# Kernel tuning notes

Hardware: AMD Instinct MI355X
Metric: run time of the kernel (lower is better)

## Reference

```python
import jax, jax.numpy as jnp
import numpy as np

N_USER = 50000
N_ITEM = 50000
E = 800000
C_IN = 128
C_OUT = 128
N_HEADS = 4


def setup_inputs() -> dict:
    key = jax.random.key(0)
    ks = jax.random.split(key, 12)
    xav = lambda k, shp: jax.random.uniform(k, shp, jnp.float32, -1.0, 1.0) * jnp.sqrt(6.0 / (shp[0] + shp[1]))
    return {
        'x_user': jax.random.normal(ks[0], (N_USER, C_IN), jnp.float32),
        'x_item': jax.random.normal(ks[1], (N_ITEM, C_IN), jnp.float32),
        'ei_u2i': jnp.stack([jax.random.randint(ks[2], (E,), 0, N_USER, jnp.int32),
                             jax.random.randint(ks[3], (E,), 0, N_ITEM, jnp.int32)]),
        'ei_i2u': jnp.stack([jax.random.randint(ks[4], (E,), 0, N_ITEM, jnp.int32),
                             jax.random.randint(ks[5], (E,), 0, N_USER, jnp.int32)]),
        'W_nb': xav(ks[6], (C_OUT, C_IN)),
        'b_nb': jnp.zeros((C_OUT,), jnp.float32),
        'W_self': xav(ks[7], (C_OUT, C_IN)),
        'b_self': jnp.zeros((C_OUT,), jnp.float32),
        'in_proj_w': xav(ks[8], (3 * C_OUT, C_OUT)),
        'in_proj_b': jnp.zeros((3 * C_OUT,), jnp.float32),
        'out_proj_w': xav(ks[9], (C_OUT, C_OUT)),
        'out_proj_b': jnp.zeros((C_OUT,), jnp.float32),
    }


def _multi_aggr(h_src, edge_index, n_dst):
    """h_src: already lin_neighbor-transformed src features [N_src, C].
    Returns [n_dst, 4, C] stacked as [max, min, sum, mean] (torch_scatter semantics:
    empty segments -> 0; mean divides by clamp(count, 1))."""
    src, dst = edge_index[0], edge_index[1]
    msgs = h_src[src]  # [E, C]  (linear commutes with gather)
    s = jax.ops.segment_sum(msgs, dst, num_segments=n_dst)
    cnt = jax.ops.segment_sum(jnp.ones((msgs.shape[0],), msgs.dtype), dst, num_segments=n_dst)
    has = (cnt > 0)[:, None]
    mean = s / jnp.maximum(cnt, 1.0)[:, None]
    mx = jnp.where(has, jax.ops.segment_max(msgs, dst, num_segments=n_dst), 0.0)
    mn = jnp.where(has, jax.ops.segment_min(msgs, dst, num_segments=n_dst), 0.0)
    return jnp.stack([mx, mn, s, mean], axis=1)  # [n_dst, 4, C]


def _mha(tokens, in_proj_w, in_proj_b, out_proj_w, out_proj_b):
    """torch nn.MultiheadAttention (eval mode, batch_first=False). tokens: [S, N, C]."""
    S, N, C = tokens.shape
    H, Dh = N_HEADS, C // N_HEADS
    qkv = tokens @ in_proj_w.T + in_proj_b            # [S, N, 3C]
    q, k, v = jnp.split(qkv, 3, axis=-1)
    q = q.reshape(S, N, H, Dh) * (1.0 / jnp.sqrt(jnp.asarray(Dh, tokens.dtype)))
    k = k.reshape(S, N, H, Dh)
    v = v.reshape(S, N, H, Dh)
    scores = jnp.einsum('snhd,tnhd->nhst', q, k)       # [N, H, S, S]
    attn = jax.nn.softmax(scores, axis=-1)
    o = jnp.einsum('nhst,tnhd->snhd', attn, v).reshape(S, N, C)
    return o @ out_proj_w.T + out_proj_b               # [S, N, C]


def reference(x_user, x_item, ei_u2i, ei_i2u, W_nb, b_nb, W_self, b_self,
              in_proj_w, in_proj_b, out_proj_w, out_proj_b):
    # shared neighbor linear applied once per node type, then gathered per edge
    h_user = x_user @ W_nb.T + b_nb
    h_item = x_item @ W_nb.T + b_nb
    aggr_item = _multi_aggr(h_user, ei_u2i, N_ITEM)    # user->item : [N_item, 4, C]
    aggr_user = _multi_aggr(h_item, ei_i2u, N_USER)    # item->user : [N_user, 4, C]

    def per_type(x, aggr):
        self_feat = x @ W_self.T + b_self              # [N, C]
        # tokens: [self, max, min, sum, mean] -> [5, N, C]
        tokens = jnp.concatenate([self_feat[None], jnp.transpose(aggr, (1, 0, 2))], axis=0)
        attn_out = _mha(tokens, in_proj_w, in_proj_b, out_proj_w, out_proj_b)
        return self_feat + attn_out.mean(axis=0)

    out_user = per_type(x_user, aggr_user)
    out_item = per_type(x_item, aggr_item)
    return (out_user, out_item)
```

## Files before the change

kernel.cpp:

```cpp
#include <hip/hip_runtime.h>
#include <hip/hip_bf16.h>


#define C 128
#define NHEAD 4
#define DH 32
#define QK_SCALE 0.17677669529663687f

typedef __attribute__((ext_vector_type(8))) short bf16x8;
typedef __attribute__((ext_vector_type(4))) short short4v;
typedef __attribute__((ext_vector_type(2))) short short2v;
typedef __attribute__((ext_vector_type(4))) float f32x4;

__device__ __forceinline__ short f2bf(float f) {
    unsigned u = __float_as_uint(f);
    unsigned r = u + 0x7FFFu + ((u >> 16) & 1u);
    return (short)(r >> 16);
}

__global__ __launch_bounds__(256, 2) void transform_prep_kernel(
    const float* __restrict__ xu, const float* __restrict__ xi,
    int NU, int NTOT,
    const float* __restrict__ Wnb, const float* __restrict__ bnb,
    const float* __restrict__ Wself, const float* __restrict__ bself,
    unsigned short* __restrict__ h_bf, unsigned short* __restrict__ self_bf,
    float* __restrict__ selfout,
    const float* __restrict__ Wip, unsigned* __restrict__ img,
    int* __restrict__ curA, int nA, int* __restrict__ curB, int nB, int TB)
{
    const int tid = threadIdx.x;

    if ((int)blockIdx.x >= TB) {
        int bid2 = (int)blockIdx.x - TB;
        if (bid2 < 96) {
            int id = bid2 * 256 + tid;
            int ks = id / (384 * 16);
            int rem = id - ks * (384 * 16);
            int n = rem >> 4, kk = rem & 15;
            float a = Wip[(size_t)n * C + ks * 32 + kk * 2 + 0];
            float b = Wip[(size_t)n * C + ks * 32 + kk * 2 + 1];
            unsigned pa = ((unsigned)(unsigned short)f2bf(a))
                        | (((unsigned)(unsigned short)f2bf(b)) << 16);
            img[(size_t)ks * 6144 + n * 16 + kk] = pa;
        } else {
            int i = (bid2 - 96) * 256 + tid;
            if (i < nA) curA[i] = 0;
            else if (i < nA + nB) curB[i - nA] = 0;
        }
        return;
    }

    __shared__ float As[64 * 132];
    __shared__ float Bs[256 * 36];
    __shared__ float biasS[256];

    const int row0 = blockIdx.x * 64;

    biasS[tid] = (tid < 128) ? bnb[tid] : bself[tid - 128];

#pragma unroll
    for (int i = 0; i < 8; i++) {
        int id = tid + i * 256;
        int r = id >> 5, c4 = id & 31;
        int row = row0 + r;
        float4 v = make_float4(0.f, 0.f, 0.f, 0.f);
        if (row < NTOT) {
            v = (row < NU) ? ((const float4*)xu)[(size_t)row * 32 + c4]
                           : ((const float4*)xi)[(size_t)(row - NU) * 32 + c4];
        }
        *(float4*)&As[r * 132 + c4 * 4] = v;
    }

    const int tm = tid >> 5;
    const int tn = tid & 31;

    float acc[8][8];
#pragma unroll
    for (int m = 0; m < 8; m++)
#pragma unroll
        for (int j = 0; j < 8; j++) acc[m][j] = 0.f;

    for (int ks = 0; ks < 4; ks++) {
        __syncthreads();
#pragma unroll
        for (int i = 0; i < 8; i++) {
            int id = tid + i * 256;
            int n = id >> 3, q = id & 7;
            const float4* src = (n < 128)
                ? &((const float4*)Wnb)[(size_t)n * 32 + ks * 8 + q]
                : &((const float4*)Wself)[(size_t)(n - 128) * 32 + ks * 8 + q];
            *(float4*)&Bs[n * 36 + q * 4] = *src;
        }
        __syncthreads();

        for (int k4 = 0; k4 < 8; k4++) {
            float4 a[8];
#pragma unroll
            for (int m = 0; m < 8; m++)
                a[m] = *(const float4*)&As[(tm * 8 + m) * 132 + ks * 32 + k4 * 4];
            float4 b[8];
#pragma unroll
            for (int j = 0; j < 8; j++)
                b[j] = *(const float4*)&Bs[(tn + 32 * j) * 36 + k4 * 4];
#pragma unroll
            for (int m = 0; m < 8; m++) {
                float4 av = a[m];
#pragma unroll
                for (int j = 0; j < 8; j++) {
                    float4 bv = b[j];
                    acc[m][j] += av.x * bv.x + av.y * bv.y
                               + av.z * bv.z + av.w * bv.w;
                }
            }
        }
    }

#pragma unroll
    for (int m = 0; m < 8; m++) {
        int row = row0 + tm * 8 + m;
        if (row < NTOT) {
#pragma unroll
            for (int j = 0; j < 8; j++) {
                int jj = tn + 32 * j;
                float v = acc[m][j] + biasS[jj];
                if (j < 4) {
                    h_bf[(size_t)row * C + jj] = (unsigned short)f2bf(v);
                } else {
                    selfout[(size_t)row * C + (jj - 128)] = v;
                    self_bf[(size_t)row * C + (jj - 128)] = (unsigned short)f2bf(v);
                }
            }
        }
    }
}

__global__ __launch_bounds__(256) void hist2_kernel(
    const int* __restrict__ dstA, int nA, int* __restrict__ curA,
    const int* __restrict__ dstB, int nB, int* __restrict__ curB)
{
    int i = blockIdx.x * 256 + threadIdx.x;
    if (i < nA) atomicAdd(&curA[dstA[i]], 1);
    else if (i < nA + nB) atomicAdd(&curB[dstB[i - nA]], 1);
}

__global__ __launch_bounds__(1024) void scan2_kernel(
    int* __restrict__ curA, int nA, int* __restrict__ curB, int nB)
{
    int* cur = (blockIdx.x == 0) ? curA : curB;
    const int n = (blockIdx.x == 0) ? nA : nB;

    __shared__ int wsum[16];
    __shared__ int carryS;
    const int tid = threadIdx.x, lane = tid & 63, wv = tid >> 6;
    if (tid == 0) carryS = 0;
    __syncthreads();
    for (int base = 0; base < n; base += 4096) {
        int i0 = base + tid * 4;
        int v0 = 0, v1 = 0, v2 = 0, v3 = 0;
        if (i0 + 3 < n) {
            int4 t = *(const int4*)&cur[i0];
            v0 = t.x; v1 = t.y; v2 = t.z; v3 = t.w;
        } else {
            if (i0 < n) v0 = cur[i0];
            if (i0 + 1 < n) v1 = cur[i0 + 1];
            if (i0 + 2 < n) v2 = cur[i0 + 2];
            if (i0 + 3 < n) v3 = cur[i0 + 3];
        }
        int s1 = v0 + v1, s2 = s1 + v2, s3 = s2 + v3;
        int x = s3;
#pragma unroll
        for (int d = 1; d < 64; d <<= 1) {
            int t = __shfl_up(x, d, 64);
            if (lane >= d) x += t;
        }
        if (lane == 63) wsum[wv] = x;
        int carry = carryS;
        __syncthreads();
        int wpre = 0;
#pragma unroll
        for (int w2 = 0; w2 < 16; w2++) wpre += (w2 < wv) ? wsum[w2] : 0;
        int excl = x - s3 + wpre + carry;
        if (i0 + 3 < n) {
            int4 st; st.x = excl; st.y = excl + v0; st.z = excl + s1; st.w = excl + s2;
            *(int4*)&cur[i0] = st;
        } else {
            if (i0 < n) cur[i0] = excl;
            if (i0 + 1 < n) cur[i0 + 1] = excl + v0;
            if (i0 + 2 < n) cur[i0 + 2] = excl + s1;
            if (i0 + 3 < n) cur[i0 + 3] = excl + s2;
        }
        __syncthreads();
        if (tid == 0) {
            int t = 0;
#pragma unroll
            for (int w2 = 0; w2 < 16; w2++) t += wsum[w2];
            carryS = carry + t;
        }
        __syncthreads();
    }
}

__global__ __launch_bounds__(256) void fill2_kernel(
    const int* __restrict__ srcA, const int* __restrict__ dstA, int nA,
    int* __restrict__ curA, unsigned short* __restrict__ csrA,
    const int* __restrict__ srcB, const int* __restrict__ dstB, int nB,
    int* __restrict__ curB, unsigned short* __restrict__ csrB)
{
    int i = blockIdx.x * 256 + threadIdx.x;
    if (i < nA) {
        int p = atomicAdd(&curA[dstA[i]], 1);
        csrA[p] = (unsigned short)srcA[i];
    } else if (i < nA + nB) {
        int j = i - nA;
        int p = atomicAdd(&curB[dstB[j]], 1);
        csrB[p] = (unsigned short)srcB[j];
    }
}

#define ATN 4

__global__ __launch_bounds__(256, 8) void attn_fused_kernel(
    const unsigned short* __restrict__ h_bf, const unsigned short* __restrict__ csr,
    const int* __restrict__ cur, const unsigned short* __restrict__ self_bf,
    const short* __restrict__ wipbf, const float* __restrict__ bip,
    float* __restrict__ omean_g, int n_nodes)
{
    __shared__ char Ash[16 * 272];
    __shared__ float cinv[ATN];

    const int tid = threadIdx.x;
    const int lane = tid & 63;
    const int wv = tid >> 6;
    const int node0 = blockIdx.x * ATN;

    if (tid < 128) {
        int r = tid >> 5, c4 = tid & 31;
        int node = node0 + r;
        short4v b = {0, 0, 0, 0};
        if (node < n_nodes)
            b = *(const short4v*)(self_bf + (size_t)node * C + c4 * 4);
        *(short4v*)(Ash + (r * 4) * 272 + c4 * 8) = b;
    }

    {
        const unsigned* h2 = (const unsigned*)h_bf;
        int node = node0 + wv;
        float2 vs = make_float2(0.f, 0.f);
        float2 vmx = make_float2(-3.4e38f, -3.4e38f);
        float2 vmn = make_float2(3.4e38f, 3.4e38f);
        int deg = 0;
        if (node < n_nodes) {
            int start = (node == 0) ? 0 : cur[node - 1];
            int end = cur[node];
            deg = end - start;
            int e = start;
            for (; e + 8 <= end; e += 8) {
                unsigned v[8];
#pragma unroll
                for (int i = 0; i < 8; i++) {
                    int s = csr[e + i];
                    v[i] = h2[(size_t)s * 64 + lane];
                }
#pragma unroll
                for (int i = 0; i < 8; i++) {
                    float fx = __uint_as_float(v[i] << 16);
                    float fy = __uint_as_float(v[i] & 0xFFFF0000u);
                    vs.x += fx; vs.y += fy;
                    vmx.x = fmaxf(vmx.x, fx); vmx.y = fmaxf(vmx.y, fy);
                    vmn.x = fminf(vmn.x, fx); vmn.y = fminf(vmn.y, fy);
                }
            }
            if (e < end) {
                int last = end - 1;
                unsigned v[8];
#pragma unroll
                for (int i = 0; i < 8; i++) {
                    int idx = e + i;
                    int s = csr[(idx <= last) ? idx : last];
                    v[i] = h2[(size_t)s * 64 + lane];
                }
#pragma unroll
                for (int i = 0; i < 8; i++) {
                    if (e + i <= last) {
                        float fx = __uint_as_float(v[i] << 16);
                        float fy = __uint_as_float(v[i] & 0xFFFF0000u);
                        vs.x += fx; vs.y += fy;
                        vmx.x = fmaxf(vmx.x, fx); vmx.y = fmaxf(vmx.y, fy);
                        vmn.x = fminf(vmn.x, fx); vmn.y = fminf(vmn.y, fy);
                    }
                }
            }
        }
        if (deg == 0) {
            vmx = make_float2(0.f, 0.f);
            vmn = make_float2(0.f, 0.f);
        }
        short2v p;
        p.x = f2bf(vmx.x); p.y = f2bf(vmx.y);
        *(short2v*)(Ash + (wv * 4 + 1) * 272 + lane * 4) = p;
        p.x = f2bf(vmn.x); p.y = f2bf(vmn.y);
        *(short2v*)(Ash + (wv * 4 + 2) * 272 + lane * 4) = p;
        p.x = f2bf(vs.x); p.y = f2bf(vs.y);
        *(short2v*)(Ash + (wv * 4 + 3) * 272 + lane * 4) = p;
        if (lane == 0) cinv[wv] = 1.f / (float)max(deg, 1);
    }
    __syncthreads();

    const int quad = lane >> 4;
    const int col16 = lane & 15;

    f32x4 acc[6];
#pragma unroll
    for (int t = 0; t < 6; t++) acc[t] = (f32x4){0.f, 0.f, 0.f, 0.f};

#pragma unroll
    for (int ks = 0; ks < 4; ks++) {
        bf16x8 af = *(const bf16x8*)(Ash + col16 * 272 + ks * 64 + quad * 16);
#pragma unroll
        for (int t = 0; t < 6; t++) {
            int nb = wv * 32 + (t & 1) * 16 + (t >> 1) * 128 + col16;
            bf16x8 bfr = *(const bf16x8*)((const char*)wipbf
                          + (size_t)ks * 24576 + (size_t)nb * 64 + quad * 16);
            acc[t] = __builtin_amdgcn_mfma_f32_16x16x32_bf16(af, bfr, acc[t], 0, 0, 0);
        }
    }

    const float ci = cinv[quad];
    const float cis = ci * QK_SCALE;

    const float bq0 = bip[wv * 32 + col16];
    const float bq1 = bip[wv * 32 + 16 + col16];
    const float bk0 = bip[128 + wv * 32 + col16];
    const float bk1 = bip[128 + wv * 32 + 16 + col16];
    const float bv0 = bip[256 + wv * 32 + col16];
    const float bv1 = bip[256 + wv * 32 + 16 + col16];
    const float bq0s = bq0 * QK_SCALE;
    const float bq1s = bq1 * QK_SCALE;

    float k0[5], k1[5];
#pragma unroll
    for (int s = 0; s < 4; s++) { k0[s] = acc[2][s] + bk0; k1[s] = acc[3][s] + bk1; }
    k0[4] = fmaf(acc[2][3], ci, bk0);
    k1[4] = fmaf(acc[3][3], ci, bk1);

    float wj[5] = {0.f, 0.f, 0.f, 0.f, 0.f};
#pragma unroll
    for (int i = 0; i < 5; i++) {
        float qi0 = (i < 4) ? fmaf(acc[0][i], QK_SCALE, bq0s)
                            : fmaf(acc[0][3], cis, bq0s);
        float qi1 = (i < 4) ? fmaf(acc[1][i], QK_SCALE, bq1s)
                            : fmaf(acc[1][3], cis, bq1s);
        float sv[5];
#pragma unroll
        for (int j = 0; j < 5; j++) sv[j] = qi0 * k0[j] + qi1 * k1[j];
#pragma unroll
        for (int j = 0; j < 5; j++) {
            sv[j] += __shfl_xor(sv[j], 1, 16);
            sv[j] += __shfl_xor(sv[j], 2, 16);
            sv[j] += __shfl_xor(sv[j], 4, 16);
            sv[j] += __shfl_xor(sv[j], 8, 16);
        }
        float m = sv[0];
#pragma unroll
        for (int j = 1; j < 5; j++) m = fmaxf(m, sv[j]);
        float e[5], l = 0.f;
#pragma unroll
        for (int j = 0; j < 5; j++) { e[j] = __expf(sv[j] - m); l += e[j]; }
        float inv = 0.2f / l;
#pragma unroll
        for (int j = 0; j < 5; j++) wj[j] = fmaf(e[j], inv, wj[j]);
    }

    float o0 = 0.f, o1 = 0.f;
#pragma unroll
    for (int j = 0; j < 5; j++) {
        float v0 = (j < 4) ? (acc[4][j] + bv0) : fmaf(acc[4][3], ci, bv0);
        float v1 = (j < 4) ? (acc[5][j] + bv1) : fmaf(acc[5][3], ci, bv1);
        o0 = fmaf(wj[j], v0, o0);
        o1 = fmaf(wj[j], v1, o1);
    }

    int node = node0 + quad;
    if (node < n_nodes) {
        omean_g[(size_t)node * C + wv * 32 + col16] = o0;
        omean_g[(size_t)node * C + wv * 32 + 16 + col16] = o1;
    }
}

__global__ __launch_bounds__(256, 3) void outproj_kernel(
    const float* __restrict__ omean_g, const float* __restrict__ Wop,
    const float* __restrict__ bop, float* __restrict__ out, int M)
{
    __shared__ float As[64 * 132];
    __shared__ float Bs[128 * 36];
    __shared__ float bopS[C];

    const int tid = threadIdx.x;
    const int m0 = blockIdx.x * 64;

    if (tid < C) bopS[tid] = bop[tid];

#pragma unroll
    for (int i = 0; i < 8; i++) {
        int id = tid + i * 256;
        int r = id >> 5, c4 = id & 31;
        float4 v = make_float4(0.f, 0.f, 0.f, 0.f);
        if (m0 + r < M) v = ((const float4*)omean_g)[(size_t)(m0 + r) * 32 + c4];
        *(float4*)&As[r * 132 + c4 * 4] = v;
    }

    const int tn = tid & 31;
    const int tm = tid >> 5;
    float acc[8][4];
#pragma unroll
    for (int m = 0; m < 8; m++)
#pragma unroll
        for (int j = 0; j < 4; j++) acc[m][j] = 0.f;

    for (int ks = 0; ks < 4; ks++) {
        __syncthreads();
#pragma unroll
        for (int i = 0; i < 4; i++) {
            int id = tid + i * 256;
            int n = id >> 3, q = id & 7;
            float4 w = ((const float4*)Wop)[(size_t)n * 32 + ks * 8 + q];
            *(float4*)&Bs[n * 36 + q * 4] = w;
        }
        __syncthreads();

        for (int k4 = 0; k4 < 8; k4++) {
            float4 a[8];
#pragma unroll
            for (int m = 0; m < 8; m++)
                a[m] = *(const float4*)&As[(tm * 8 + m) * 132 + ks * 32 + k4 * 4];
            float4 b[4];
#pragma unroll
            for (int j = 0; j < 4; j++)
                b[j] = *(const float4*)&Bs[(tn + 32 * j) * 36 + k4 * 4];
#pragma unroll
            for (int m = 0; m < 8; m++) {
                float4 av = a[m];
#pragma unroll
                for (int j = 0; j < 4; j++) {
                    float4 bv = b[j];
                    acc[m][j] += av.x * bv.x + av.y * bv.y
                               + av.z * bv.z + av.w * bv.w;
                }
            }
        }
    }

#pragma unroll
    for (int m = 0; m < 8; m++) {
        int row = m0 + tm * 8 + m;
        if (row < M) {
#pragma unroll
            for (int j = 0; j < 4; j++) {
                int col = tn + 32 * j;
                float* o = &out[(size_t)row * C + col];
                *o += acc[m][j] + bopS[col];
            }
        }
    }
}

extern "C" void kernel_launch(void* const* d_in, const int* in_sizes, int n_in,
                              void* d_out, int out_size, void* d_ws, size_t ws_size,
                              hipStream_t stream) {
    const float* x_user = (const float*)d_in[0];
    const float* x_item = (const float*)d_in[1];
    const int*   ei_u2i = (const int*)d_in[2];
    const int*   ei_i2u = (const int*)d_in[3];
    const float* W_nb   = (const float*)d_in[4];
    const float* b_nb   = (const float*)d_in[5];
    const float* W_self = (const float*)d_in[6];
    const float* b_self = (const float*)d_in[7];
    const float* Wip    = (const float*)d_in[8];
    const float* bip    = (const float*)d_in[9];
    const float* Wop    = (const float*)d_in[10];
    const float* bop    = (const float*)d_in[11];

    const int NU = in_sizes[0] / C;
    const int NI = in_sizes[1] / C;
    const int E1 = in_sizes[2] / 2;
    const int E2 = in_sizes[3] / 2;
    const int NTOT = NU + NI;

    float* out_user = (float*)d_out;
    float* out_item = out_user + (size_t)NU * C;

    float* ws = (float*)d_ws;
    short* wipbf            = (short*)ws;
    unsigned short* h_bf    = (unsigned short*)(ws + 24576);
    const size_t rc = (size_t)NTOT * C;
    unsigned short* self_bf = h_bf + rc;
    float* omean_all        = (float*)(self_bf + rc);
    int*   curA             = (int*)(omean_all + rc);
    int*   curB             = curA + NI;
    unsigned short* csrA16  = (unsigned short*)(curB + NU);
    unsigned short* csrB16  = csrA16 + E1;

    unsigned short* h_user_bf = h_bf;
    unsigned short* h_item_bf = h_bf + (size_t)NU * C;
    unsigned short* self_user_bf = self_bf;
    unsigned short* self_item_bf = self_bf + (size_t)NU * C;
    float* om_user = omean_all;
    float* om_item = omean_all + (size_t)NU * C;

    const int TB = (NTOT + 63) / 64;
    const int PB = 96 + (NTOT + 255) / 256;
    transform_prep_kernel<<<TB + PB, 256, 0, stream>>>(
        x_user, x_item, NU, NTOT, W_nb, b_nb, W_self, b_self,
        h_bf, self_bf, (float*)d_out, Wip, (unsigned*)wipbf,
        curA, NI, curB, NU, TB);

    hist2_kernel<<<(E1 + E2 + 255) / 256, 256, 0, stream>>>(
        ei_u2i + E1, E1, curA, ei_i2u + E2, E2, curB);

    scan2_kernel<<<2, 1024, 0, stream>>>(curA, NI, curB, NU);

    fill2_kernel<<<(E1 + E2 + 255) / 256, 256, 0, stream>>>(
        ei_u2i, ei_u2i + E1, E1, curA, csrA16,
        ei_i2u, ei_i2u + E2, E2, curB, csrB16);

    attn_fused_kernel<<<(NU + ATN - 1) / ATN, 256, 0, stream>>>(
        h_item_bf, csrB16, curB, self_user_bf, wipbf, bip, om_user, NU);

    attn_fused_kernel<<<(NI + ATN - 1) / ATN, 256, 0, stream>>>(
        h_user_bf, csrA16, curA, self_item_bf, wipbf, bip, om_item, NI);

    outproj_kernel<<<(NTOT + 63) / 64, 256, 0, stream>>>(
        omean_all, Wop, bop, (float*)d_out, NTOT);
}
```

Measured before the change: 672.8 us.

## Use bf16 MFMA for node linear transforms with pre-packed weight image

```diff
diff --git a/kernel.cpp b/kernel.cpp
--- a/kernel.cpp
+++ b/kernel.cpp
@@ -18,42 +18,57 @@
     return (short)(r >> 16);
 }
 
-__global__ __launch_bounds__(256, 2) void transform_prep_kernel(
+__global__ __launch_bounds__(256) void prep_kernel(
+    const float* __restrict__ Wip, unsigned* __restrict__ img,
+    const float* __restrict__ Wnb, const float* __restrict__ Wself,
+    unsigned* __restrict__ imgW,
+    int* __restrict__ curA, int nA, int* __restrict__ curB, int nB)
+{
+    const int tid = threadIdx.x;
+    const int bid = (int)blockIdx.x;
+    if (bid < 96) {
+        int id = bid * 256 + tid;
+        int ks = id / (384 * 16);
+        int rem = id - ks * (384 * 16);
+        int n = rem >> 4, kk = rem & 15;
+        float a = Wip[(size_t)n * C + ks * 32 + kk * 2 + 0];
+        float b = Wip[(size_t)n * C + ks * 32 + kk * 2 + 1];
+        unsigned pa = ((unsigned)(unsigned short)f2bf(a))
+                    | (((unsigned)(unsigned short)f2bf(b)) << 16);
+        img[(size_t)ks * 6144 + n * 16 + kk] = pa;
+    } else if (bid < 160) {
+        int id = (bid - 96) * 256 + tid;
+        int ks = id / (256 * 16);
+        int rem = id - ks * (256 * 16);
+        int n = rem >> 4, kk = rem & 15;
+        const float* src = (n < 128) ? &Wnb[(size_t)n * C]
+                                     : &Wself[(size_t)(n - 128) * C];
+        float a = src[ks * 32 + kk * 2 + 0];
+        float b = src[ks * 32 + kk * 2 + 1];
+        unsigned pa = ((unsigned)(unsigned short)f2bf(a))
+                    | (((unsigned)(unsigned short)f2bf(b)) << 16);
+        imgW[(size_t)ks * 4096 + n * 16 + kk] = pa;
+    } else {
+        int i = (bid - 160) * 256 + tid;
+        if (i < nA) curA[i] = 0;
+        else if (i < nA + nB) curB[i - nA] = 0;
+    }
+}
+
+__global__ __launch_bounds__(256, 4) void transform_kernel(
     const float* __restrict__ xu, const float* __restrict__ xi,
     int NU, int NTOT,
-    const float* __restrict__ Wnb, const float* __restrict__ bnb,
-    const float* __restrict__ Wself, const float* __restrict__ bself,
+    const unsigned short* __restrict__ wnsbf,
+    const float* __restrict__ bnb, const float* __restrict__ bself,
     unsigned short* __restrict__ h_bf, unsigned short* __restrict__ self_bf,
-    float* __restrict__ selfout,
-    const float* __restrict__ Wip, unsigned* __restrict__ img,
-    int* __restrict__ curA, int nA, int* __restrict__ curB, int nB, int TB)
-{
+    float* __restrict__ selfout)
+{
+    __shared__ char Ash[64 * 272];
+    __shared__ float biasS[256];
+
     const int tid = threadIdx.x;
-
-    if ((int)blockIdx.x >= TB) {
-        int bid2 = (int)blockIdx.x - TB;
-        if (bid2 < 96) {
-            int id = bid2 * 256 + tid;
-            int ks = id / (384 * 16);
-            int rem = id - ks * (384 * 16);
-            int n = rem >> 4, kk = rem & 15;
-            float a = Wip[(size_t)n * C + ks * 32 + kk * 2 + 0];
-            float b = Wip[(size_t)n * C + ks * 32 + kk * 2 + 1];
-            unsigned pa = ((unsigned)(unsigned short)f2bf(a))
-                        | (((unsigned)(unsigned short)f2bf(b)) << 16);
-            img[(size_t)ks * 6144 + n * 16 + kk] = pa;
-        } else {
-            int i = (bid2 - 96) * 256 + tid;
-            if (i < nA) curA[i] = 0;
-            else if (i < nA + nB) curB[i - nA] = 0;
-        }
-        return;
-    }
-
-    __shared__ float As[64 * 132];
-    __shared__ float Bs[256 * 36];
-    __shared__ float biasS[256];
-
+    const int lane = tid & 63;
+    const int wv = tid >> 6;
     const int row0 = blockIdx.x * 64;
 
     biasS[tid] = (tid < 128) ? bnb[tid] : bself[tid - 128];
@@ -68,66 +83,57 @@
             v = (row < NU) ? ((const float4*)xu)[(size_t)row * 32 + c4]
                            : ((const float4*)xi)[(size_t)(row - NU) * 32 + c4];
         }
-        *(float4*)&As[r * 132 + c4 * 4] = v;
-    }
-
-    const int tm = tid >> 5;
-    const int tn = tid & 31;
-
-    float acc[8][8];
-#pragma unroll
-    for (int m = 0; m < 8; m++)
-#pragma unroll
-        for (int j = 0; j < 8; j++) acc[m][j] = 0.f;
-
+        short4v b;
+        b.x = f2bf(v.x); b.y = f2bf(v.y); b.z = f2bf(v.z); b.w = f2bf(v.w);
+        *(short4v*)(Ash + r * 272 + c4 * 8) = b;
+    }
+    __syncthreads();
+
+    const int quad = lane >> 4;
+    const int col16 = lane & 15;
+
+    f32x4 acc[4][4];
+#pragma unroll
+    for (int mt = 0; mt < 4; mt++)
+#pragma unroll
+        for (int nt = 0; nt < 4; nt++) acc[mt][nt] = (f32x4){0.f, 0.f, 0.f, 0.f};
+
+#pragma unroll
     for (int ks = 0; ks < 4; ks++) {
-        __syncthreads();
-#pragma unroll
-        for (int i = 0; i < 8; i++) {
-            int id = tid + i * 256;
-            int n = id >> 3, q = id & 7;
-            const float4* src = (n < 128)
-                ? &((const float4*)Wnb)[(size_t)n * 32 + ks * 8 + q]
-                : &((const float4*)Wself)[(size_t)(n - 128) * 32 + ks * 8 + q];
-            *(float4*)&Bs[n * 36 + q * 4] = *src;
-        }
-        __syncthreads();
-
-        for (int k4 = 0; k4 < 8; k4++) {
-            float4 a[8];
-#pragma unroll
-            for (int m = 0; m < 8; m++)
-                a[m] = *(const float4*)&As[(tm * 8 + m) * 132 + ks * 32 + k4 * 4];
-            float4 b[8];
-#pragma unroll
-            for (int j = 0; j < 8; j++)
-                b[j] = *(const float4*)&Bs[(tn + 32 * j) * 36 + k4 * 4];
-#pragma unroll
-            for (int m = 0; m < 8; m++) {
-                float4 av = a[m];
-#pragma unroll
-                for (int j = 0; j < 8; j++) {
-                    float4 bv = b[j];
-                    acc[m][j] += av.x * bv.x + av.y * bv.y
-                               + av.z * bv.z + av.w * bv.w;
-                }
-            }
-        }
-    }
-
-#pragma unroll
-    for (int m = 0; m < 8; m++) {
-        int row = row0 + tm * 8 + m;
-        if (row < NTOT) {
-#pragma unroll
-            for (int j = 0; j < 8; j++) {
-                int jj = tn + 32 * j;
-                float v = acc[m][j] + biasS[jj];
-                if (j < 4) {
-                    h_bf[(size_t)row * C + jj] = (unsigned short)f2bf(v);
-                } else {
-                    selfout[(size_t)row * C + (jj - 128)] = v;
-                    self_bf[(size_t)row * C + (jj - 128)] = (unsigned short)f2bf(v);
+        bf16x8 bfv[4];
+#pragma unroll
+        for (int nt = 0; nt < 4; nt++) {
+            int n = (wv * 4 + nt) * 16 + col16;
+            bfv[nt] = *(const bf16x8*)((const char*)wnsbf
+                        + (size_t)ks * 16384 + (size_t)n * 64 + quad * 16);
+        }
+#pragma unroll
+        for (int mt = 0; mt < 4; mt++) {
+            bf16x8 af = *(const bf16x8*)(Ash + (mt * 16 + col16) * 272
+                                         + ks * 64 + quad * 16);
+#pragma unroll
+            for (int nt = 0; nt < 4; nt++)
+                acc[mt][nt] = __builtin_amdgcn_mfma_f32_16x16x32_bf16(
+                                  af, bfv[nt], acc[mt][nt], 0, 0, 0);
+        }
+    }
+
+#pragma unroll
+    for (int mt = 0; mt < 4; mt++) {
+#pragma unroll
+        for (int reg = 0; reg < 4; reg++) {
+            int row = row0 + mt * 16 + quad * 4 + reg;
+            if (row < NTOT) {
+#pragma unroll
+                for (int nt = 0; nt < 4; nt++) {
+                    int col = (wv * 4 + nt) * 16 + col16;
+                    float v = acc[mt][nt][reg] + biasS[col];
+                    if (wv < 2) {
+                        h_bf[(size_t)row * C + col] = (unsigned short)f2bf(v);
+                    } else {
+                        selfout[(size_t)row * C + (col - 128)] = v;
+                        self_bf[(size_t)row * C + (col - 128)] = (unsigned short)f2bf(v);
+                    }
                 }
             }
         }
@@ -486,12 +492,10 @@
     const int E2 = in_sizes[3] / 2;
     const int NTOT = NU + NI;
 
-    float* out_user = (float*)d_out;
-    float* out_item = out_user + (size_t)NU * C;
-
     float* ws = (float*)d_ws;
     short* wipbf            = (short*)ws;
-    unsigned short* h_bf    = (unsigned short*)(ws + 24576);
+    unsigned short* wnsbf   = (unsigned short*)(ws + 24576);
+    unsigned short* h_bf    = (unsigned short*)(ws + 24576 + 16384);
     const size_t rc = (size_t)NTOT * C;
     unsigned short* self_bf = h_bf + rc;
     float* omean_all        = (float*)(self_bf + rc);
@@ -507,12 +511,13 @@
     float* om_user = omean_all;
     float* om_item = omean_all + (size_t)NU * C;
 
-    const int TB = (NTOT + 63) / 64;
-    const int PB = 96 + (NTOT + 255) / 256;
-    transform_prep_kernel<<<TB + PB, 256, 0, stream>>>(
-        x_user, x_item, NU, NTOT, W_nb, b_nb, W_self, b_self,
-        h_bf, self_bf, (float*)d_out, Wip, (unsigned*)wipbf,
-        curA, NI, curB, NU, TB);
+    prep_kernel<<<160 + (NTOT + 255) / 256, 256, 0, stream>>>(
+        Wip, (unsigned*)wipbf, W_nb, W_self, (unsigned*)wnsbf,
+        curA, NI, curB, NU);
+
+    transform_kernel<<<(NTOT + 63) / 64, 256, 0, stream>>>(
+        x_user, x_item, NU, NTOT, wnsbf, b_nb, b_self,
+        h_bf, self_bf, (float*)d_out);
 
     hist2_kernel<<<(E1 + E2 + 255) / 256, 256, 0, stream>>>(
         ei_u2i + E1, E1, curA, ei_i2u + E2, E2, curB);
```

Result: faster. 603.3 us (-10.3%).
